# Kernel optimization log

Measured on AMD Instinct MI355X. Metric: run time of the kernel, lower is better.

The kernel has to match this reference:

```python
import jax, jax.numpy as jnp
import numpy as np

NEG = -1e9  # finite stand-in for -inf (keeps gradients NaN-free)
BLANK_LOGPROB = -1.0


def _lse(*xs):
    m = xs[0]
    for x in xs[1:]:
        m = jnp.maximum(m, x)
    s = sum(jnp.exp(x - m) for x in xs)
    return m + jnp.log(s)


def _forward_sum_loss(attn_logprob, text_lens, mel_lens):
    # attn_logprob: [B, 1, T, U]; text/mel lens: [B] int
    B, _, T, U = attn_logprob.shape
    x = attn_logprob[:, 0]                                   # [B, T, U]
    # pad a blank column at text index 0 (F.pad(..., (1,0,...)), value=blank_logprob)
    x = jnp.pad(x, ((0, 0), (0, 0), (1, 0)), constant_values=BLANK_LOGPROB)  # [B,T,U+1]
    # per-sample log_softmax over only the first text_len+1 columns (matches the
    # torch slice [:, :, :text_len+1] before LogSoftmax) -> mask padding columns
    cols = jnp.arange(U + 1)
    valid_col = cols[None, :] <= text_lens[:, None]          # [B, U+1]
    x = jnp.where(valid_col[:, None, :], x, NEG)
    lp = jax.nn.log_softmax(x, axis=-1)                      # [B, T, U+1]

    # CTC forward-sum. Target for sample b is [1, 2, ..., text_len_b] (all
    # distinct labels), extended with blanks: s=0..2U, label(s)=0 if s even else (s+1)//2.
    S = 2 * U + 1
    s = jnp.arange(S)
    lab = jnp.where(s % 2 == 0, 0, (s + 1) // 2)             # [S]
    odd = (s % 2 == 1)
    lp_ext = lp[:, :, lab]                                   # [B, T, S]
    # columns beyond text_len are NEG after log_softmax, so invalid label
    # positions (odd s with (s+1)//2 > text_len) are automatically killed.

    idx_last = 2 * text_lens                                 # [B] final blank position
    neg1 = jnp.full((B, 1), NEG, lp.dtype)
    neg2 = jnp.full((B, 2), NEG, lp.dtype)

    def step(alpha, lp_t):
        a1 = alpha                                           # stay
        a2 = jnp.concatenate([neg1, alpha[:, :-1]], axis=1)  # advance 1
        a3 = jnp.concatenate([neg2, alpha[:, :-2]], axis=1)  # skip (labels distinct)
        a3 = jnp.where(odd[None, :], a3, NEG)                # skip only into label positions
        new = lp_t + _lse(a1, a2, a3)                        # [B, S]
        fin = _lse(jnp.take_along_axis(new, idx_last[:, None], axis=1)[:, 0],
                   jnp.take_along_axis(new, (idx_last - 1)[:, None], axis=1)[:, 0])
        return new, fin

    alpha0 = jnp.full((B, S), NEG, lp.dtype).at[:, 0].set(0.0)
    lp_ts = jnp.transpose(lp_ext, (1, 0, 2))                 # [T, B, S]
    _, fins = jax.lax.scan(step, alpha0, lp_ts)              # [T, B]
    final = jnp.take_along_axis(fins, (mel_lens - 1)[None, :], axis=0)[0]  # [B]
    # nn.CTCLoss(reduction='mean') on a batch of 1 divides by target length;
    # zero_infinity zeroes out impossible alignments.
    loss = jnp.where(final < NEG / 2, 0.0, -final / text_lens.astype(lp.dtype))
    return jnp.mean(loss)


def setup_inputs() -> dict:
    key = jax.random.key(0)
    k1, k2, k3 = jax.random.split(key, 3)
    B, T, U = 64, 1000, 250
    attn_logprob = jax.random.normal(k1, (B, 1, T, U), dtype=jnp.float32)
    text_lens = jax.random.randint(k2, (B,), 50, U + 1, dtype=jnp.int32)
    mel_lens = jax.random.randint(k3, (B,), 600, T + 1, dtype=jnp.int32)
    return {"attn_logprob": attn_logprob, "text_lens": text_lens, "mel_lens": mel_lens}


def reference(attn_logprob, text_lens, mel_lens):
    return _forward_sum_loss(attn_logprob, text_lens, mel_lens)
```

## Files before the change

kernel.cpp:

```cpp
#include <hip/hip_runtime.h>

#define NEGF -1000000000.0f
#define LOG2E 1.4426950408889634f
#define LN2 0.6931471805599453f

constexpr int Bn = 64;
constexpr int Tn = 1000;
constexpr int Un = 250;

__device__ __forceinline__ float exp2fast(float x) { return __builtin_amdgcn_exp2f(x); }
__device__ __forceinline__ float log2fast(float x) { return __builtin_amdgcn_logf(x); }

template <int CTRL>
__device__ __forceinline__ float dppmov(float x) {
    return __int_as_float(__builtin_amdgcn_update_dpp(
        0, __float_as_int(x), CTRL, 0xf, 0xf, true));
}
__device__ __forceinline__ float dpp_wave_shr1(float x) { return dppmov<0x138>(x); }

__device__ __forceinline__ float wave_red_max(float x) {
    x = fmaxf(x, dppmov<0x111>(x));
    x = fmaxf(x, dppmov<0x112>(x));
    x = fmaxf(x, dppmov<0x114>(x));
    x = fmaxf(x, dppmov<0x118>(x));
    x = fmaxf(x, dppmov<0x142>(x));
    x = fmaxf(x, dppmov<0x143>(x));
    return __int_as_float(__builtin_amdgcn_readlane(__float_as_int(x), 63));
}
__device__ __forceinline__ float wave_red_sum(float x) {
    x += dppmov<0x111>(x);
    x += dppmov<0x112>(x);
    x += dppmov<0x114>(x);
    x += dppmov<0x118>(x);
    x += dppmov<0x142>(x);
    x += dppmov<0x143>(x);
    return __int_as_float(__builtin_amdgcn_readlane(__float_as_int(x), 63));
}

__global__ void __launch_bounds__(256) zrow_kernel(const float* __restrict__ attn,
                                                   const int* __restrict__ text_lens,
                                                   float* __restrict__ Z2,
                                                   float* __restrict__ out) {
    if (blockIdx.x == 0 && threadIdx.x == 0) *out = 0.0f;
    int wid = threadIdx.x >> 6;
    int lane = threadIdx.x & 63;
    int row0 = (blockIdx.x * 4 + wid) * 4;

    float v[4][4];
    int Ls[4];
#pragma unroll
    for (int r = 0; r < 4; ++r) {
        int row = row0 + r;
        Ls[r] = text_lens[row / Tn];
        const float* p = attn + (size_t)row * Un;
#pragma unroll
        for (int i = 0; i < 4; ++i) {
            int u = lane + 64 * i;
            v[r][i] = (u < Un) ? p[u] : 0.0f;
        }
    }
#pragma unroll
    for (int r = 0; r < 4; ++r) {
        int L = Ls[r];
        float m = (lane == 0) ? -LOG2E : NEGF;
#pragma unroll
        for (int i = 0; i < 4; ++i) {
            int u = lane + 64 * i;
            v[r][i] = (u < L) ? v[r][i] * LOG2E : NEGF;
            m = fmaxf(m, v[r][i]);
        }
        m = wave_red_max(m);
        float s = (lane == 0) ? exp2fast(-LOG2E - m) : 0.0f;
#pragma unroll
        for (int i = 0; i < 4; ++i) s += exp2fast(v[r][i] - m);
        s = wave_red_sum(s);
        if (lane == 0) Z2[row0 + r] = m + log2fast(s);
    }
}

typedef float v2f __attribute__((ext_vector_type(2)));

#define CTC_REFILL(J, T)                                                      \
    {                                                                         \
        int tl_ = (T) <= last ? (T) : last;                                   \
        const char* rowp_ = pbase + (size_t)tl_ * 1000;                       \
        asm volatile("global_load_dwordx2 %0, %1, %2"                         \
                     : "=v"(lo[J]) : "v"(voff_lo), "s"(rowp_));               \
        asm volatile("global_load_dwordx2 %0, %1, %2"                         \
                     : "=v"(hi[J]) : "v"(voff_hi), "s"(rowp_));               \
    }

#define CTC_STEP(J, WCNT)                                                     \
    {                                                                         \
        asm volatile("s_waitcnt vmcnt(" #WCNT ")"                             \
                     : "+v"(lo[J]), "+v"(hi[J]));                             \
        float q0 = exp2fast(__builtin_fmaf(lo[J].x, LOG2E, bias0));           \
        float q1 = exp2fast(__builtin_fmaf(lo[J].y, LOG2E, bias1));           \
        float q2 = exp2fast(__builtin_fmaf(hi[J].x, LOG2E, bias2));           \
        float q3 = exp2fast(__builtin_fmaf(hi[J].y, LOG2E, bias3));           \
        float p7 = dpp_wave_shr1(a7);       \
        float s65 = a6 + a5, s43 = a4 + a3, s21 = a2 + a1, s0p = a0 + p7;     \
        a7 = (a7 + s65) * q3;  a6 = s65 * QB;                                 \
        a5 = (a5 + s43) * q2;  a4 = s43 * QB;                                 \
        a3 = (a3 + s21) * q1;  a2 = s21 * QB;                                 \
        a1 = (a1 + s0p) * q0;  a0 = s0p * QB;                                 \
    }

#define RENORM()                                                              \
    {                                                                         \
        float mx = fmaxf(fmaxf(fmaxf(a0, a1), fmaxf(a2, a3)),                 \
                         fmaxf(fmaxf(a4, a5), fmaxf(a6, a7)));                \
        mx = wave_red_max(mx);                \
        int e_ = (int)((__float_as_uint(mx) >> 23) & 255) - 127;              \
        float scale_ = __uint_as_float((unsigned)(127 - e_) << 23);           \
        a0 *= scale_; a1 *= scale_; a2 *= scale_; a3 *= scale_;               \
        a4 *= scale_; a5 *= scale_; a6 *= scale_; a7 *= scale_;               \
        Esum += (float)e_;                                                    \
    }

__global__ void __launch_bounds__(64, 1) ctc_kernel(const float* __restrict__ attn,
                                                    const int* __restrict__ text_lens,
                                                    const int* __restrict__ mel_lens,
                                                    const float* __restrict__ Z2,
                                                    float* __restrict__ out) {
    int b = blockIdx.x;
    int lane = threadIdx.x;
    int L = text_lens[b];
    int n_t = mel_lens[b];
    const char* pbase = (const char*)(attn + (size_t)b * Tn * Un);

    int voff_lo = lane * 16, voff_hi = lane * 16 + 8;
    if (lane == 62) { voff_lo = 992; voff_hi = 992; }
    if (lane == 63) { voff_lo = 0;   voff_hi = 0;   }
    int c0 = lane * 4;
    float bias0 = (c0 + 0 < L) ? 0.0f : -1000000.0f;
    float bias1 = (c0 + 1 < L) ? 0.0f : -1000000.0f;
    float bias2 = (c0 + 2 < L) ? 0.0f : -1000000.0f;
    float bias3 = (c0 + 3 < L) ? 0.0f : -1000000.0f;

    const float QB = 0.36787944117144233f;
    float a0 = (lane == 0) ? 1.0f : 0.0f;
    float a1 = 0.0f, a2 = 0.0f, a3 = 0.0f, a4 = 0.0f, a5 = 0.0f, a6 = 0.0f, a7 = 0.0f;
    float Esum = 0.0f;

    v2f lo[16], hi[16];
    int last = n_t - 1;

#pragma unroll
    for (int j = 0; j < 16; ++j) CTC_REFILL(j, j);

    int full = n_t & ~15;
    int t = 0;
    for (; t < full; t += 16) {
        CTC_STEP(0, 30);  CTC_REFILL(0, t + 16);
        CTC_STEP(1, 30);  CTC_REFILL(1, t + 17);
        CTC_STEP(2, 30);  CTC_REFILL(2, t + 18);
        CTC_STEP(3, 30);  CTC_REFILL(3, t + 19);
        CTC_STEP(4, 30);  CTC_REFILL(4, t + 20);
        CTC_STEP(5, 30);  CTC_REFILL(5, t + 21);
        CTC_STEP(6, 30);  CTC_REFILL(6, t + 22);
        CTC_STEP(7, 30);  CTC_REFILL(7, t + 23);
        RENORM();
        CTC_STEP(8, 30);  CTC_REFILL(8, t + 24);
        CTC_STEP(9, 30);  CTC_REFILL(9, t + 25);
        CTC_STEP(10, 30); CTC_REFILL(10, t + 26);
        CTC_STEP(11, 30); CTC_REFILL(11, t + 27);
        CTC_STEP(12, 30); CTC_REFILL(12, t + 28);
        CTC_STEP(13, 30); CTC_REFILL(13, t + 29);
        CTC_STEP(14, 30); CTC_REFILL(14, t + 30);
        CTC_STEP(15, 30); CTC_REFILL(15, t + 31);
        RENORM();
    }
    if (t + 0 < n_t) CTC_STEP(0, 0);
    if (t + 1 < n_t) CTC_STEP(1, 0);
    if (t + 2 < n_t) CTC_STEP(2, 0);
    if (t + 3 < n_t) CTC_STEP(3, 0);
    if (t + 4 < n_t) CTC_STEP(4, 0);
    if (t + 5 < n_t) CTC_STEP(5, 0);
    if (t + 6 < n_t) CTC_STEP(6, 0);
    if (t + 7 < n_t) CTC_STEP(7, 0);
    if (t + 8 < n_t) { RENORM(); CTC_STEP(8, 0); }
    if (t + 9 < n_t) CTC_STEP(9, 0);
    if (t + 10 < n_t) CTC_STEP(10, 0);
    if (t + 11 < n_t) CTC_STEP(11, 0);
    if (t + 12 < n_t) CTC_STEP(12, 0);
    if (t + 13 < n_t) CTC_STEP(13, 0);
    if (t + 14 < n_t) CTC_STEP(14, 0);
    asm volatile("s_waitcnt vmcnt(0)" ::: "memory");

    __shared__ float sal[512];
    sal[lane * 8 + 0] = a0;
    sal[lane * 8 + 1] = a1;
    sal[lane * 8 + 2] = a2;
    sal[lane * 8 + 3] = a3;
    sal[lane * 8 + 4] = a4;
    sal[lane * 8 + 5] = a5;
    sal[lane * 8 + 6] = a6;
    sal[lane * 8 + 7] = a7;
    __syncthreads();

    float zs = 0.0f;
    for (int i = lane; i < n_t; i += 64) zs += Z2[b * Tn + i];
    zs = wave_red_sum(zs);

    if (lane == 0) {
        float ssum = sal[2 * L] + sal[2 * L - 1];
        float fin = (log2fast(ssum) + Esum - zs) * LN2;
        float loss = (ssum <= 0.0f) ? 0.0f : (-fin / (float)L);
        atomicAdd(out, loss * (1.0f / (float)Bn));
    }
}

extern "C" void kernel_launch(void* const* d_in, const int* in_sizes, int n_in,
                              void* d_out, int out_size, void* d_ws, size_t ws_size,
                              hipStream_t stream) {
    const float* attn = (const float*)d_in[0];
    const int* text_lens = (const int*)d_in[1];
    const int* mel_lens = (const int*)d_in[2];
    float* out = (float*)d_out;
    float* Z2 = (float*)d_ws;

    zrow_kernel<<<Bn * Tn / 16, 256, 0, stream>>>(attn, text_lens, Z2, out);
    ctc_kernel<<<Bn, 64, 0, stream>>>(attn, text_lens, mel_lens, Z2, out);
}
```

Baseline: 175.5 us.

## Software-pipeline exp2 emission factor generation eight steps ahead of the recurrence

Splits each CTC step into an emission-factor stage (wait for the load, then fma+exp2) and a recurrence stage. The factors for the next eight time steps are computed into register arrays ahead of time. Load buffers are recycled one stage earlier, so the exp2 latency no longer sits on the serial alpha dependency chain. This adds about 32 live VGPRs and a more intricate prologue and epilogue, where a wrong vmcnt or slot assignment would give incorrect results.

```diff
diff --git a/kernel.cpp b/kernel.cpp
--- a/kernel.cpp
+++ b/kernel.cpp
@@ -90,14 +90,19 @@
                      : "=v"(hi[J]) : "v"(voff_hi), "s"(rowp_));               \
     }
 
-#define CTC_STEP(J, WCNT)                                                     \
+#define QGEN(Q, S, WCNT)                                                      \
     {                                                                         \
         asm volatile("s_waitcnt vmcnt(" #WCNT ")"                             \
-                     : "+v"(lo[J]), "+v"(hi[J]));                             \
-        float q0 = exp2fast(__builtin_fmaf(lo[J].x, LOG2E, bias0));           \
-        float q1 = exp2fast(__builtin_fmaf(lo[J].y, LOG2E, bias1));           \
-        float q2 = exp2fast(__builtin_fmaf(hi[J].x, LOG2E, bias2));           \
-        float q3 = exp2fast(__builtin_fmaf(hi[J].y, LOG2E, bias3));           \
+                     : "+v"(lo[S]), "+v"(hi[S]));                             \
+        qa[Q] = exp2fast(__builtin_fmaf(lo[S].x, LOG2E, bias0));              \
+        qb[Q] = exp2fast(__builtin_fmaf(lo[S].y, LOG2E, bias1));              \
+        qc[Q] = exp2fast(__builtin_fmaf(hi[S].x, LOG2E, bias2));              \
+        qd[Q] = exp2fast(__builtin_fmaf(hi[S].y, LOG2E, bias3));              \
+    }
+
+#define STEP_Q(Q)                                                             \
+    {                                                                         \
+        float q0 = qa[Q], q1 = qb[Q], q2 = qc[Q], q3 = qd[Q];                 \
         float p7 = dpp_wave_shr1(a7);       \
         float s65 = a6 + a5, s43 = a4 + a3, s21 = a2 + a1, s0p = a0 + p7;     \
         a7 = (a7 + s65) * q3;  a6 = s65 * QB;                                 \
@@ -144,48 +149,53 @@
     float Esum = 0.0f;
 
     v2f lo[16], hi[16];
+    float qa[8], qb[8], qc[8], qd[8];
     int last = n_t - 1;
 
 #pragma unroll
     for (int j = 0; j < 16; ++j) CTC_REFILL(j, j);
+    QGEN(0, 0, 30); QGEN(1, 1, 28); QGEN(2, 2, 26); QGEN(3, 3, 24);
+    QGEN(4, 4, 22); QGEN(5, 5, 20); QGEN(6, 6, 18); QGEN(7, 7, 16);
+#pragma unroll
+    for (int j = 0; j < 8; ++j) CTC_REFILL(j, 16 + j);
 
     int full = n_t & ~15;
     int t = 0;
     for (; t < full; t += 16) {
-        CTC_STEP(0, 30);  CTC_REFILL(0, t + 16);
-        CTC_STEP(1, 30);  CTC_REFILL(1, t + 17);
-        CTC_STEP(2, 30);  CTC_REFILL(2, t + 18);
-        CTC_STEP(3, 30);  CTC_REFILL(3, t + 19);
-        CTC_STEP(4, 30);  CTC_REFILL(4, t + 20);
-        CTC_STEP(5, 30);  CTC_REFILL(5, t + 21);
-        CTC_STEP(6, 30);  CTC_REFILL(6, t + 22);
-        CTC_STEP(7, 30);  CTC_REFILL(7, t + 23);
+        STEP_Q(0); QGEN(0, 8, 30);  CTC_REFILL(8,  t + 24);
+        STEP_Q(1); QGEN(1, 9, 30);  CTC_REFILL(9,  t + 25);
+        STEP_Q(2); QGEN(2, 10, 30); CTC_REFILL(10, t + 26);
+        STEP_Q(3); QGEN(3, 11, 30); CTC_REFILL(11, t + 27);
+        STEP_Q(4); QGEN(4, 12, 30); CTC_REFILL(12, t + 28);
+        STEP_Q(5); QGEN(5, 13, 30); CTC_REFILL(13, t + 29);
+        STEP_Q(6); QGEN(6, 14, 30); CTC_REFILL(14, t + 30);
+        STEP_Q(7); QGEN(7, 15, 30); CTC_REFILL(15, t + 31);
         RENORM();
-        CTC_STEP(8, 30);  CTC_REFILL(8, t + 24);
-        CTC_STEP(9, 30);  CTC_REFILL(9, t + 25);
-        CTC_STEP(10, 30); CTC_REFILL(10, t + 26);
-        CTC_STEP(11, 30); CTC_REFILL(11, t + 27);
-        CTC_STEP(12, 30); CTC_REFILL(12, t + 28);
-        CTC_STEP(13, 30); CTC_REFILL(13, t + 29);
-        CTC_STEP(14, 30); CTC_REFILL(14, t + 30);
-        CTC_STEP(15, 30); CTC_REFILL(15, t + 31);
+        STEP_Q(0); QGEN(0, 0, 30);  CTC_REFILL(0, t + 32);
+        STEP_Q(1); QGEN(1, 1, 30);  CTC_REFILL(1, t + 33);
+        STEP_Q(2); QGEN(2, 2, 30);  CTC_REFILL(2, t + 34);
+        STEP_Q(3); QGEN(3, 3, 30);  CTC_REFILL(3, t + 35);
+        STEP_Q(4); QGEN(4, 4, 30);  CTC_REFILL(4, t + 36);
+        STEP_Q(5); QGEN(5, 5, 30);  CTC_REFILL(5, t + 37);
+        STEP_Q(6); QGEN(6, 6, 30);  CTC_REFILL(6, t + 38);
+        STEP_Q(7); QGEN(7, 7, 30);  CTC_REFILL(7, t + 39);
         RENORM();
     }
-    if (t + 0 < n_t) CTC_STEP(0, 0);
-    if (t + 1 < n_t) CTC_STEP(1, 0);
-    if (t + 2 < n_t) CTC_STEP(2, 0);
-    if (t + 3 < n_t) CTC_STEP(3, 0);
-    if (t + 4 < n_t) CTC_STEP(4, 0);
-    if (t + 5 < n_t) CTC_STEP(5, 0);
-    if (t + 6 < n_t) CTC_STEP(6, 0);
-    if (t + 7 < n_t) CTC_STEP(7, 0);
-    if (t + 8 < n_t) { RENORM(); CTC_STEP(8, 0); }
-    if (t + 9 < n_t) CTC_STEP(9, 0);
-    if (t + 10 < n_t) CTC_STEP(10, 0);
-    if (t + 11 < n_t) CTC_STEP(11, 0);
-    if (t + 12 < n_t) CTC_STEP(12, 0);
-    if (t + 13 < n_t) CTC_STEP(13, 0);
-    if (t + 14 < n_t) CTC_STEP(14, 0);
+    if (t + 0 < n_t) STEP_Q(0);
+    if (t + 1 < n_t) STEP_Q(1);
+    if (t + 2 < n_t) STEP_Q(2);
+    if (t + 3 < n_t) STEP_Q(3);
+    if (t + 4 < n_t) STEP_Q(4);
+    if (t + 5 < n_t) STEP_Q(5);
+    if (t + 6 < n_t) STEP_Q(6);
+    if (t + 7 < n_t) STEP_Q(7);
+    if (t + 8 < n_t)  { RENORM(); QGEN(0, 8, 0); STEP_Q(0); }
+    if (t + 9 < n_t)  { QGEN(1, 9, 0);  STEP_Q(1); }
+    if (t + 10 < n_t) { QGEN(2, 10, 0); STEP_Q(2); }
+    if (t + 11 < n_t) { QGEN(3, 11, 0); STEP_Q(3); }
+    if (t + 12 < n_t) { QGEN(4, 12, 0); STEP_Q(4); }
+    if (t + 13 < n_t) { QGEN(5, 13, 0); STEP_Q(5); }
+    if (t + 14 < n_t) { QGEN(6, 14, 0); STEP_Q(6); }
     asm volatile("s_waitcnt vmcnt(0)" ::: "memory");
 
     __shared__ float sal[512];
```

After: 172.0 us. About the same (-2.0%).

## Fuse row normalizer into CTC kernel with producer-consumer waves via LDS ring

Applied to the files above, without the earlier changes.

Removes the separate row log-sum-exp kernel. Each CTC block now has three producer waves and one consumer wave. The producers load rows, compute the exponentiated emission factors and per-row partition sums, and pass them to the consumer through a shared-memory ring buffer guarded by ready and done flags. The consumer wave runs only the alpha recurrence from LDS, taking the exps and global-load latency off its serial path and saving a second full pass over the input. The cost is spin-wait synchronisation, LDS read latency on every step, and the risk of subtle ordering bugs in the hand-built flag protocol.

```diff
diff --git a/kernel.cpp b/kernel.cpp
--- a/kernel.cpp
+++ b/kernel.cpp
@@ -7,6 +7,7 @@
 constexpr int Bn = 64;
 constexpr int Tn = 1000;
 constexpr int Un = 250;
+constexpr int RING_GRPS = 12;
 
 __device__ __forceinline__ float exp2fast(float x) { return __builtin_amdgcn_exp2f(x); }
 __device__ __forceinline__ float log2fast(float x) { return __builtin_amdgcn_logf(x); }
@@ -37,52 +38,12 @@
     return __int_as_float(__builtin_amdgcn_readlane(__float_as_int(x), 63));
 }
 
-__global__ void __launch_bounds__(256) zrow_kernel(const float* __restrict__ attn,
-                                                   const int* __restrict__ text_lens,
-                                                   float* __restrict__ Z2,
-                                                   float* __restrict__ out) {
-    if (blockIdx.x == 0 && threadIdx.x == 0) *out = 0.0f;
-    int wid = threadIdx.x >> 6;
-    int lane = threadIdx.x & 63;
-    int row0 = (blockIdx.x * 4 + wid) * 4;
-
-    float v[4][4];
-    int Ls[4];
-#pragma unroll
-    for (int r = 0; r < 4; ++r) {
-        int row = row0 + r;
-        Ls[r] = text_lens[row / Tn];
-        const float* p = attn + (size_t)row * Un;
-#pragma unroll
-        for (int i = 0; i < 4; ++i) {
-            int u = lane + 64 * i;
-            v[r][i] = (u < Un) ? p[u] : 0.0f;
-        }
-    }
-#pragma unroll
-    for (int r = 0; r < 4; ++r) {
-        int L = Ls[r];
-        float m = (lane == 0) ? -LOG2E : NEGF;
-#pragma unroll
-        for (int i = 0; i < 4; ++i) {
-            int u = lane + 64 * i;
-            v[r][i] = (u < L) ? v[r][i] * LOG2E : NEGF;
-            m = fmaxf(m, v[r][i]);
-        }
-        m = wave_red_max(m);
-        float s = (lane == 0) ? exp2fast(-LOG2E - m) : 0.0f;
-#pragma unroll
-        for (int i = 0; i < 4; ++i) s += exp2fast(v[r][i] - m);
-        s = wave_red_sum(s);
-        if (lane == 0) Z2[row0 + r] = m + log2fast(s);
-    }
-}
-
 typedef float v2f __attribute__((ext_vector_type(2)));
 
-#define CTC_REFILL(J, T)                                                      \
+#define PREFILL(J, T)                                                         \
     {                                                                         \
         int tl_ = (T) <= last ? (T) : last;                                   \
+        tl_ = __builtin_amdgcn_readfirstlane(tl_);                            \
         const char* rowp_ = pbase + (size_t)tl_ * 1000;                       \
         asm volatile("global_load_dwordx2 %0, %1, %2"                         \
                      : "=v"(lo[J]) : "v"(voff_lo), "s"(rowp_));               \
@@ -90,20 +51,48 @@
                      : "=v"(hi[J]) : "v"(voff_hi), "s"(rowp_));               \
     }
 
-#define CTC_STEP(J, WCNT)                                                     \
-    {                                                                         \
-        asm volatile("s_waitcnt vmcnt(" #WCNT ")"                             \
-                     : "+v"(lo[J]), "+v"(hi[J]));                             \
-        float q0 = exp2fast(__builtin_fmaf(lo[J].x, LOG2E, bias0));           \
-        float q1 = exp2fast(__builtin_fmaf(lo[J].y, LOG2E, bias1));           \
-        float q2 = exp2fast(__builtin_fmaf(hi[J].x, LOG2E, bias2));           \
-        float q3 = exp2fast(__builtin_fmaf(hi[J].y, LOG2E, bias3));           \
+#define PROW(SLOT, J)                                                         \
+    {                                                                         \
+        asm volatile("s_waitcnt vmcnt(30)"                                    \
+                     : "+v"(lo[SLOT]), "+v"(hi[SLOT]));                       \
+        float q0 = exp2fast(__builtin_fmaf(lo[SLOT].x, LOG2E, bias0));        \
+        float q1 = exp2fast(__builtin_fmaf(lo[SLOT].y, LOG2E, bias1));        \
+        float q2 = exp2fast(__builtin_fmaf(hi[SLOT].x, LOG2E, bias2));        \
+        float q3 = exp2fast(__builtin_fmaf(hi[SLOT].y, LOG2E, bias3));        \
+        int row_ = 8 * g + (J);                                               \
+        if (row_ < n_t) {                                                     \
+            float4 qv_; qv_.x = q0; qv_.y = q1; qv_.z = q2; qv_.w = q3;       \
+            *(float4*)(rb_ + (J) * 256) = qv_;                                \
+            float rs_ = wave_red_sum((q0 + q1) + (q2 + q3));                  \
+            zacc += log2fast(QB + rs_);                                       \
+        }                                                                     \
+        PREFILL(SLOT, row_ + 48);                                             \
+    }
+
+#define PGRP(SB)                                                              \
+    {                                                                         \
+        if (g >= RING_GRPS) {                                                 \
+            while (__hip_atomic_load(&cons_done, __ATOMIC_ACQUIRE,            \
+                       __HIP_MEMORY_SCOPE_WORKGROUP) < g - RING_GRPS + 1)     \
+                __builtin_amdgcn_s_sleep(1);                                  \
+        }                                                                     \
+        float* rb_ = &ring[(size_t)(g % RING_GRPS) * 2048 + lane * 4];        \
+        PROW(SB + 0, 0); PROW(SB + 1, 1); PROW(SB + 2, 2); PROW(SB + 3, 3);   \
+        PROW(SB + 4, 4); PROW(SB + 5, 5); PROW(SB + 6, 6); PROW(SB + 7, 7);   \
+        asm volatile("s_waitcnt lgkmcnt(0)" ::: "memory");                    \
+        __hip_atomic_store(&ready[g % RING_GRPS], g + 1, __ATOMIC_RELEASE,    \
+                           __HIP_MEMORY_SCOPE_WORKGROUP);                     \
+    }
+
+#define CSTEP(J)                                                              \
+    {                                                                         \
+        float4 qv_ = *(const float4*)(rb_ + (J) * 256);                       \
         float p7 = dpp_wave_shr1(a7);       \
         float s65 = a6 + a5, s43 = a4 + a3, s21 = a2 + a1, s0p = a0 + p7;     \
-        a7 = (a7 + s65) * q3;  a6 = s65 * QB;                                 \
-        a5 = (a5 + s43) * q2;  a4 = s43 * QB;                                 \
-        a3 = (a3 + s21) * q1;  a2 = s21 * QB;                                 \
-        a1 = (a1 + s0p) * q0;  a0 = s0p * QB;                                 \
+        a7 = (a7 + s65) * qv_.w;  a6 = s65 * QB;                              \
+        a5 = (a5 + s43) * qv_.z;  a4 = s43 * QB;                              \
+        a3 = (a3 + s21) * qv_.y;  a2 = s21 * QB;                              \
+        a1 = (a1 + s0p) * qv_.x;  a0 = s0p * QB;                              \
     }
 
 #define RENORM()                                                              \
@@ -118,16 +107,28 @@
         Esum += (float)e_;                                                    \
     }
 
-__global__ void __launch_bounds__(64, 1) ctc_kernel(const float* __restrict__ attn,
-                                                    const int* __restrict__ text_lens,
-                                                    const int* __restrict__ mel_lens,
-                                                    const float* __restrict__ Z2,
-                                                    float* __restrict__ out) {
+__global__ void __launch_bounds__(256, 1) ctc_pc_kernel(
+        const float* __restrict__ attn,
+        const int* __restrict__ text_lens,
+        const int* __restrict__ mel_lens,
+        float* __restrict__ out) {
+    __shared__ float ring[RING_GRPS * 8 * 256];
+    __shared__ int ready[RING_GRPS];
+    __shared__ int cons_done;
+    __shared__ float sal[512];
+    __shared__ float zparts[3];
+
     int b = blockIdx.x;
-    int lane = threadIdx.x;
+    int wid = threadIdx.x >> 6;
+    int lane = threadIdx.x & 63;
     int L = text_lens[b];
     int n_t = mel_lens[b];
     const char* pbase = (const char*)(attn + (size_t)b * Tn * Un);
+    int G = (n_t + 7) >> 3;
+
+    if (threadIdx.x < RING_GRPS) ready[threadIdx.x] = 0;
+    if (threadIdx.x == RING_GRPS) cons_done = 0;
+    __syncthreads();
 
     int voff_lo = lane * 16, voff_hi = lane * 16 + 8;
     if (lane == 62) { voff_lo = 992; voff_hi = 992; }
@@ -139,71 +140,67 @@
     float bias3 = (c0 + 3 < L) ? 0.0f : -1000000.0f;
 
     const float QB = 0.36787944117144233f;
-    float a0 = (lane == 0) ? 1.0f : 0.0f;
-    float a1 = 0.0f, a2 = 0.0f, a3 = 0.0f, a4 = 0.0f, a5 = 0.0f, a6 = 0.0f, a7 = 0.0f;
     float Esum = 0.0f;
 
-    v2f lo[16], hi[16];
-    int last = n_t - 1;
+    if (wid == 0) {
+        float a0 = (lane == 0) ? 1.0f : 0.0f;
+        float a1 = 0.0f, a2 = 0.0f, a3 = 0.0f, a4 = 0.0f, a5 = 0.0f,
+              a6 = 0.0f, a7 = 0.0f;
+        for (int g = 0; g < G; ++g) {
+            int s = g % RING_GRPS;
+            while (__hip_atomic_load(&ready[s], __ATOMIC_ACQUIRE,
+                       __HIP_MEMORY_SCOPE_WORKGROUP) != g + 1)
+                __builtin_amdgcn_s_sleep(1);
+            __builtin_amdgcn_sched_barrier(0);
+            const float* rb_ = &ring[(size_t)s * 2048 + lane * 4];
+            int base_ = 8 * g;
+            if (base_ + 0 < n_t) CSTEP(0);
+            if (base_ + 1 < n_t) CSTEP(1);
+            if (base_ + 2 < n_t) CSTEP(2);
+            if (base_ + 3 < n_t) CSTEP(3);
+            if (base_ + 4 < n_t) CSTEP(4);
+            if (base_ + 5 < n_t) CSTEP(5);
+            if (base_ + 6 < n_t) CSTEP(6);
+            if (base_ + 7 < n_t) CSTEP(7);
+            RENORM();
+            __hip_atomic_store(&cons_done, g + 1, __ATOMIC_RELEASE,
+                               __HIP_MEMORY_SCOPE_WORKGROUP);
+        }
+        sal[lane * 8 + 0] = a0;
+        sal[lane * 8 + 1] = a1;
+        sal[lane * 8 + 2] = a2;
+        sal[lane * 8 + 3] = a3;
+        sal[lane * 8 + 4] = a4;
+        sal[lane * 8 + 5] = a5;
+        sal[lane * 8 + 6] = a6;
+        sal[lane * 8 + 7] = a7;
+    } else {
+        float zacc = 0.0f;
+        v2f lo[16], hi[16];
+        int last = n_t - 1;
+        int g = wid - 1;
+        int ng = (G - (wid - 1) + 2) / 3;
 
 #pragma unroll
-    for (int j = 0; j < 16; ++j) CTC_REFILL(j, j);
-
-    int full = n_t & ~15;
-    int t = 0;
-    for (; t < full; t += 16) {
-        CTC_STEP(0, 30);  CTC_REFILL(0, t + 16);
-        CTC_STEP(1, 30);  CTC_REFILL(1, t + 17);
-        CTC_STEP(2, 30);  CTC_REFILL(2, t + 18);
-        CTC_STEP(3, 30);  CTC_REFILL(3, t + 19);
-        CTC_STEP(4, 30);  CTC_REFILL(4, t + 20);
-        CTC_STEP(5, 30);  CTC_REFILL(5, t + 21);
-        CTC_STEP(6, 30);  CTC_REFILL(6, t + 22);
-        CTC_STEP(7, 30);  CTC_REFILL(7, t + 23);
-        RENORM();
-        CTC_STEP(8, 30);  CTC_REFILL(8, t + 24);
-        CTC_STEP(9, 30);  CTC_REFILL(9, t + 25);
-        CTC_STEP(10, 30); CTC_REFILL(10, t + 26);
-        CTC_STEP(11, 30); CTC_REFILL(11, t + 27);
-        CTC_STEP(12, 30); CTC_REFILL(12, t + 28);
-        CTC_STEP(13, 30); CTC_REFILL(13, t + 29);
-        CTC_STEP(14, 30); CTC_REFILL(14, t + 30);
-        CTC_STEP(15, 30); CTC_REFILL(15, t + 31);
-        RENORM();
-    }
-    if (t + 0 < n_t) CTC_STEP(0, 0);
-    if (t + 1 < n_t) CTC_STEP(1, 0);
-    if (t + 2 < n_t) CTC_STEP(2, 0);
-    if (t + 3 < n_t) CTC_STEP(3, 0);
-    if (t + 4 < n_t) CTC_STEP(4, 0);
-    if (t + 5 < n_t) CTC_STEP(5, 0);
-    if (t + 6 < n_t) CTC_STEP(6, 0);
-    if (t + 7 < n_t) CTC_STEP(7, 0);
-    if (t + 8 < n_t) { RENORM(); CTC_STEP(8, 0); }
-    if (t + 9 < n_t) CTC_STEP(9, 0);
-    if (t + 10 < n_t) CTC_STEP(10, 0);
-    if (t + 11 < n_t) CTC_STEP(11, 0);
-    if (t + 12 < n_t) CTC_STEP(12, 0);
-    if (t + 13 < n_t) CTC_STEP(13, 0);
-    if (t + 14 < n_t) CTC_STEP(14, 0);
-    asm volatile("s_waitcnt vmcnt(0)" ::: "memory");
-
-    __shared__ float sal[512];
-    sal[lane * 8 + 0] = a0;
-    sal[lane * 8 + 1] = a1;
-    sal[lane * 8 + 2] = a2;
-    sal[lane * 8 + 3] = a3;
-    sal[lane * 8 + 4] = a4;
-    sal[lane * 8 + 5] = a5;
-    sal[lane * 8 + 6] = a6;
-    sal[lane * 8 + 7] = a7;
+        for (int j = 0; j < 16; ++j) {
+            int r0_ = 8 * g + 24 * (j >> 3) + (j & 7);
+            PREFILL(j, r0_);
+        }
+        int gk = 0;
+        while (true) {
+            PGRP(0);
+            ++gk; g += 3; if (gk == ng) break;
+            PGRP(8);
+            ++gk; g += 3; if (gk == ng) break;
+        }
+        asm volatile("s_waitcnt vmcnt(0)" ::: "memory");
+        if (lane == 0) zparts[wid - 1] = zacc;
+    }
+
     __syncthreads();
 
-    float zs = 0.0f;
-    for (int i = lane; i < n_t; i += 64) zs += Z2[b * Tn + i];
-    zs = wave_red_sum(zs);
-
-    if (lane == 0) {
+    if (threadIdx.x == 0) {
+        float zs = zparts[0] + zparts[1] + zparts[2];
         float ssum = sal[2 * L] + sal[2 * L - 1];
         float fin = (log2fast(ssum) + Esum - zs) * LN2;
         float loss = (ssum <= 0.0f) ? 0.0f : (-fin / (float)L);
@@ -218,8 +215,7 @@
     const int* text_lens = (const int*)d_in[1];
     const int* mel_lens = (const int*)d_in[2];
     float* out = (float*)d_out;
-    float* Z2 = (float*)d_ws;
-
-    zrow_kernel<<<Bn * Tn / 16, 256, 0, stream>>>(attn, text_lens, Z2, out);
-    ctc_kernel<<<Bn, 64, 0, stream>>>(attn, text_lens, mel_lens, Z2, out);
-}
+
+    hipMemsetAsync(out, 0, sizeof(float), stream);
+    ctc_pc_kernel<<<Bn, 256, 0, stream>>>(attn, text_lens, mel_lens, out);
+}
```

Result: faster. 166.1 us (-5.3%).
